# Performance work log

Measured on AMD Instinct MI355X. Metric: run time of the kernel, lower is better.

Reference implementation:

```python
import jax, jax.numpy as jnp
import numpy as np

D_MODEL = 1024
NUM_HEADS = 16
D_K = D_MODEL // NUM_HEADS
BATCH = 4
SEQ = 1024
NEG_INF = jnp.float32(-1e30)


def setup_inputs() -> dict:
    key = jax.random.key(0)
    ks = jax.random.split(key, 12)
    s = 1.0 / np.sqrt(D_MODEL)
    inp = {
        "Q": jax.random.normal(ks[0], (BATCH, SEQ, D_MODEL), jnp.float32),
        "K": jax.random.normal(ks[1], (BATCH, SEQ, D_MODEL), jnp.float32),
        "V": jax.random.normal(ks[2], (BATCH, SEQ, D_MODEL), jnp.float32),
        # causal mask, broadcastable [1,1,Sq,Sk]; entries==0 are masked out
        "mask": jnp.tril(jnp.ones((SEQ, SEQ), jnp.int32))[None, None],
        "W_q": jax.random.normal(ks[3], (D_MODEL, D_MODEL), jnp.float32) * s,
        "b_q": jnp.zeros((D_MODEL,), jnp.float32),
        "W_k": jax.random.normal(ks[4], (D_MODEL, D_MODEL), jnp.float32) * s,
        "b_k": jnp.zeros((D_MODEL,), jnp.float32),
        "W_v": jax.random.normal(ks[5], (D_MODEL, D_MODEL), jnp.float32) * s,
        "b_v": jnp.zeros((D_MODEL,), jnp.float32),
        "W_o": jax.random.normal(ks[6], (D_MODEL, D_MODEL), jnp.float32) * s,
        "b_o": jnp.zeros((D_MODEL,), jnp.float32),
    }
    return inp


def _split_heads(x):
    b, s, _ = x.shape
    return x.reshape(b, s, NUM_HEADS, D_K).transpose(0, 2, 1, 3)  # [b,h,s,dk]


def reference(Q, K, V, mask, W_q, b_q, W_k, b_k, W_v, b_v, W_o, b_o):
    # linear projections (torch Linear: x @ W.T + b)
    q = _split_heads(Q @ W_q.T + b_q)
    k = _split_heads(K @ W_k.T + b_k)
    v = _split_heads(V @ W_v.T + b_v)
    scale = 1.0 / jnp.sqrt(jnp.float32(D_K))
    scores = jnp.einsum("bhqd,bhkd->bhqk", q, k) * scale
    scores = jnp.where(mask == 0, NEG_INF, scores)
    attn = jax.nn.softmax(scores, axis=-1)  # dropout is identity in eval mode
    out = jnp.einsum("bhqk,bhkd->bhqd", attn, v)
    out = out.transpose(0, 2, 1, 3).reshape(Q.shape[0], Q.shape[1], D_MODEL)
    out = out @ W_o.T + b_o
    return out, attn
```

## Files before the change

### kernel.cpp

```cpp
#include <hip/hip_runtime.h>
#include <math.h>

#define SEQ 1024
#define DM  1024

typedef unsigned short u16;
typedef __attribute__((ext_vector_type(8))) short bf16x8;
typedef __attribute__((ext_vector_type(8))) unsigned short u16x8;
typedef __attribute__((ext_vector_type(4))) float f32x4;

__device__ __forceinline__ u16 f2bf(float f) {
  union { float f; unsigned int u; } x; x.f = f;
  return (u16)((x.u + 0x7fffu + ((x.u >> 16) & 1u)) >> 16);
}

__device__ __forceinline__ void gload16(const void* g, void* l) {
  __builtin_amdgcn_global_load_lds(
      (const __attribute__((address_space(1))) unsigned int*)g,
      (__attribute__((address_space(3))) unsigned int*)l, 16, 0, 0);
}

struct ConvArgs { const float* s[7]; u16* d[7]; };

__global__ __launch_bounds__(256) void conv_bf16(ConvArgs a) {
  const long long t  = (long long)blockIdx.x * 256 + threadIdx.x;
  const long long e0 = t * 8;
  const int u   = (int)(e0 >> 20);
  const int seg = (u < 12) ? (u >> 2) : (u - 9);
  const long long base = (u < 12) ? ((long long)(u >> 2) << 22) : ((long long)u << 20);
  const long long off  = e0 - base;
  const float* sp = a.s[seg] + off;
  float4 x = *(const float4*)sp;
  float4 y = *(const float4*)(sp + 4);
  u16x8 o;
  o[0]=f2bf(x.x); o[1]=f2bf(x.y); o[2]=f2bf(x.z); o[3]=f2bf(x.w);
  o[4]=f2bf(y.x); o[5]=f2bf(y.y); o[6]=f2bf(y.z); o[7]=f2bf(y.w);
  *(u16x8*)(a.d[seg] + off) = o;
}

struct GemmJob  { const u16* X; const u16* W; const float* bias; void* out; int mode; float scale; };
struct GemmJobs { GemmJob j[3]; };

__global__ __launch_bounds__(256) void gemm_bt(GemmJobs jobs) {
  __shared__ u16 As[8192];
  __shared__ u16 Bs[8192];
  const GemmJob job = jobs.j[blockIdx.z];
  const int tid  = threadIdx.x;
  const int wave = tid >> 6, lane = tid & 63;
  const int lm = lane & 15, qd = lane >> 4;
  const int wm = wave & 1,  wn = wave >> 1;
  const int tm = blockIdx.x * 128, tn = blockIdx.y * 128;

  f32x4 acc[4][4];
  #pragma unroll
  for (int i = 0; i < 4; i++)
    #pragma unroll
    for (int jx = 0; jx < 4; jx++) { f32x4 z = {0.f,0.f,0.f,0.f}; acc[i][jx] = z; }

  for (int kt = 0; kt < 1024; kt += 64) {
    #pragma unroll
    for (int i = 0; i < 4; i++) {
      const int s = (wave * 4 + i) * 64 + lane;
      const int r = s >> 3;
      const int c = (s & 7) ^ (r & 7);
      gload16(job.X + (size_t)(tm + r) * 1024 + kt + c * 8, As + (wave * 4 + i) * 512);
      gload16(job.W + (size_t)(tn + r) * 1024 + kt + c * 8, Bs + (wave * 4 + i) * 512);
    }
    __syncthreads();
    #pragma unroll
    for (int ks = 0; ks < 2; ks++) {
      bf16x8 af[4], bf[4];
      #pragma unroll
      for (int i = 0; i < 4; i++) {
        const int ra = wm * 64 + i * 16 + lm;
        af[i] = *(const bf16x8*)&As[ra * 64 + ((((ks << 2) | qd)) ^ (ra & 7)) * 8];
        const int rb = wn * 64 + i * 16 + lm;
        bf[i] = *(const bf16x8*)&Bs[rb * 64 + ((((ks << 2) | qd)) ^ (rb & 7)) * 8];
      }
      #pragma unroll
      for (int mi = 0; mi < 4; mi++)
        #pragma unroll
        for (int ni = 0; ni < 4; ni++)
          acc[mi][ni] = __builtin_amdgcn_mfma_f32_16x16x32_bf16(af[mi], bf[ni], acc[mi][ni], 0, 0, 0);
    }
    __syncthreads();
  }

  #pragma unroll
  for (int ni = 0; ni < 4; ni++) {
    const int n = tn + wn * 64 + ni * 16 + lm;
    const float bn = job.bias[n];
    #pragma unroll
    for (int mi = 0; mi < 4; mi++) {
      #pragma unroll
      for (int r = 0; r < 4; r++) {
        const int m = tm + wm * 64 + mi * 16 + (qd << 2) + r;
        const float v = (acc[mi][ni][r] + bn) * job.scale;
        if (job.mode == 0) {
          const int b = m >> 10, s = m & 1023, h = n >> 6, d = n & 63;
          ((u16*)job.out)[((size_t)((b << 4) + h) * 1024 + s) * 64 + d] = f2bf(v);
        } else if (job.mode == 1) {
          const int b = m >> 10, s = m & 1023, h = n >> 6, d = n & 63;
          ((u16*)job.out)[((size_t)((b << 4) + h) * 64 + d) * 1024 + s] = f2bf(v);
        } else {
          ((float*)job.out)[(size_t)m * 1024 + n] = v;
        }
      }
    }
  }
}

__global__ __launch_bounds__(256)
void attn_pass1(const u16* __restrict__ qbuf, const u16* __restrict__ kbuf,
                const u16* __restrict__ vtbuf, float* __restrict__ Linv,
                u16* __restrict__ ctx) {
  __shared__ u16 P[4][512];
  const int tid = threadIdx.x, wave = tid >> 6, lane = tid & 63;
  const int lm = lane & 15, qd = lane >> 4;
  const int qt = blockIdx.x * 4 + wave;
  const int bh = blockIdx.y;
  const int q0 = qt * 16;
  const u16* Q  = qbuf  + (size_t)bh * SEQ * 64;
  const u16* K  = kbuf  + (size_t)bh * SEQ * 64;
  const u16* VT = vtbuf + (size_t)bh * 64 * SEQ;

  const bf16x8 qa = *(const bf16x8*)(Q + (size_t)(q0 + lm) * 64 + qd * 8);
  const bf16x8 qb = *(const bf16x8*)(Q + (size_t)(q0 + lm) * 64 + 32 + qd * 8);

  f32x4 o[4];
  float lsum[4] = {0.f, 0.f, 0.f, 0.f};
  #pragma unroll
  for (int i = 0; i < 4; i++) { f32x4 z = {0.f,0.f,0.f,0.f}; o[i] = z; }
  u16* Pw = P[wave];

  for (int kt = 0; kt < q0 + 16; kt += 32) {
    const u16* k0p = K + (size_t)(kt + lm) * 64 + qd * 8;
    const u16* k1p = K + (size_t)(kt + 16 + lm) * 64 + qd * 8;
    const bf16x8 k0a = *(const bf16x8*)k0p;
    const bf16x8 k0b = *(const bf16x8*)(k0p + 32);
    const bf16x8 k1a = *(const bf16x8*)k1p;
    const bf16x8 k1b = *(const bf16x8*)(k1p + 32);
    f32x4 s0 = {0.f,0.f,0.f,0.f}, s1 = {0.f,0.f,0.f,0.f};
    s0 = __builtin_amdgcn_mfma_f32_16x16x32_bf16(qa, k0a, s0, 0, 0, 0);
    s0 = __builtin_amdgcn_mfma_f32_16x16x32_bf16(qb, k0b, s0, 0, 0, 0);
    s1 = __builtin_amdgcn_mfma_f32_16x16x32_bf16(qa, k1a, s1, 0, 0, 0);
    s1 = __builtin_amdgcn_mfma_f32_16x16x32_bf16(qb, k1b, s1, 0, 0, 0);
    #pragma unroll
    for (int r = 0; r < 4; r++) {
      const int row = q0 + (qd << 2) + r;
      const float e0 = (kt + lm      <= row) ? __expf(s0[r]) : 0.f;
      const float e1 = (kt + 16 + lm <= row) ? __expf(s1[r]) : 0.f;
      lsum[r] += e0 + e1;
      Pw[((qd << 2) + r) * 32 + lm]      = f2bf(e0);
      Pw[((qd << 2) + r) * 32 + 16 + lm] = f2bf(e1);
    }
    const bf16x8 pf = *(const bf16x8*)&Pw[lm * 32 + qd * 8];
    #pragma unroll
    for (int db = 0; db < 4; db++) {
      const bf16x8 vf = *(const bf16x8*)(VT + (size_t)(db * 16 + lm) * SEQ + kt + qd * 8);
      o[db] = __builtin_amdgcn_mfma_f32_16x16x32_bf16(pf, vf, o[db], 0, 0, 0);
    }
  }

  const int b = bh >> 4, h = bh & 15;
  #pragma unroll
  for (int r = 0; r < 4; r++) {
    float l = lsum[r];
    l += __shfl_xor(l, 1, 16);
    l += __shfl_xor(l, 2, 16);
    l += __shfl_xor(l, 4, 16);
    l += __shfl_xor(l, 8, 16);
    const float inv = 1.0f / l;
    const int row = q0 + (qd << 2) + r;
    if (lm == 0) Linv[(size_t)bh * SEQ + row] = inv;
    #pragma unroll
    for (int db = 0; db < 4; db++) {
      const int d = db * 16 + lm;
      ctx[(size_t)(b * SEQ + row) * DM + h * 64 + d] = f2bf(o[db][r] * inv);
    }
  }
}

__global__ __launch_bounds__(256)
void attn_pass2(const u16* __restrict__ qbuf, const u16* __restrict__ kbuf,
                const float* __restrict__ Linv, float* __restrict__ attn) {
  const int tid = threadIdx.x, wave = tid >> 6, lane = tid & 63;
  const int lm = lane & 15, qd = lane >> 4;
  const int bh = blockIdx.z;
  const int q0 = blockIdx.y * 64;
  const int k0 = blockIdx.x * 256 + wave * 64;
  float* A = attn + (size_t)bh * SEQ * SEQ;

  if (k0 > q0 + 63) {
    const f32x4 z = {0.f,0.f,0.f,0.f};
    #pragma unroll
    for (int i = 0; i < 16; i++)
      *(f32x4*)&A[(size_t)(q0 + i * 4 + qd) * SEQ + k0 + lm * 4] = z;
    return;
  }

  const u16* Q = qbuf + (size_t)bh * SEQ * 64;
  const u16* K = kbuf + (size_t)bh * SEQ * 64;
  bf16x8 qf[4][2]; float invl[4];
  #pragma unroll
  for (int qs = 0; qs < 4; qs++) {
    const int qq = q0 + qs * 16;
    qf[qs][0] = *(const bf16x8*)(Q + (size_t)(qq + lm) * 64 + qd * 8);
    qf[qs][1] = *(const bf16x8*)(Q + (size_t)(qq + lm) * 64 + 32 + qd * 8);
    invl[qs]  = Linv[(size_t)bh * SEQ + qq + lm];
  }
  for (int ks = 0; ks < 4; ks++) {
    const int kk = k0 + ks * 16;
    const u16* kp = K + (size_t)(kk + lm) * 64 + qd * 8;
    const bf16x8 kf0 = *(const bf16x8*)kp;
    const bf16x8 kf1 = *(const bf16x8*)(kp + 32);
    #pragma unroll
    for (int qs = 0; qs < 4; qs++) {
      const int qq = q0 + qs * 16;
      const int kbase = kk + (qd << 2);
      f32x4 v = {0.f,0.f,0.f,0.f};
      if (kk <= qq + 15) {
        f32x4 c = {0.f,0.f,0.f,0.f};
        c = __builtin_amdgcn_mfma_f32_16x16x32_bf16(kf0, qf[qs][0], c, 0, 0, 0);
        c = __builtin_amdgcn_mfma_f32_16x16x32_bf16(kf1, qf[qs][1], c, 0, 0, 0);
        const int qg = qq + lm;
        #pragma unroll
        for (int r = 0; r < 4; r++)
          v[r] = (kbase + r <= qg) ? __expf(c[r]) * invl[qs] : 0.f;
      }
      *(f32x4*)&A[(size_t)(qq + lm) * SEQ + kbase] = v;
    }
  }
}

extern "C" void kernel_launch(void* const* d_in, const int* in_sizes, int n_in,
                              void* d_out, int out_size, void* d_ws, size_t ws_size,
                              hipStream_t stream)
{
  (void)in_sizes; (void)n_in; (void)out_size; (void)ws_size;
  const float* Qf = (const float*)d_in[0];
  const float* Kf = (const float*)d_in[1];
  const float* Vf = (const float*)d_in[2];
  const float* Wq = (const float*)d_in[4];
  const float* bq = (const float*)d_in[5];
  const float* Wk = (const float*)d_in[6];
  const float* bk = (const float*)d_in[7];
  const float* Wv = (const float*)d_in[8];
  const float* bv = (const float*)d_in[9];
  const float* Wo = (const float*)d_in[10];
  const float* bo = (const float*)d_in[11];

  float* out  = (float*)d_out;
  float* attn = out + (size_t)4 * SEQ * DM;

  char* sc = (char*)attn;
  u16* Xq  = (u16*)(sc);
  u16* Xk  = (u16*)(sc + (8  << 20));
  u16* Xv  = (u16*)(sc + (16 << 20));
  u16* Wqb = (u16*)(sc + (24 << 20));
  u16* Wkb = (u16*)(sc + (26 << 20));
  u16* Wvb = (u16*)(sc + (28 << 20));
  u16* Wob = (u16*)(sc + (30 << 20));
  u16* ctx = (u16*)(sc + (32 << 20));

  char* ws   = (char*)d_ws;
  u16* qbuf  = (u16*)ws;
  u16* kbuf  = (u16*)(ws + (8  << 20));
  u16* vtbuf = (u16*)(ws + (16 << 20));
  float* Linv = (float*)(ws + (24 << 20));

  ConvArgs ca;
  ca.s[0]=Qf; ca.s[1]=Kf; ca.s[2]=Vf; ca.s[3]=Wq; ca.s[4]=Wk; ca.s[5]=Wv; ca.s[6]=Wo;
  ca.d[0]=Xq; ca.d[1]=Xk; ca.d[2]=Xv; ca.d[3]=Wqb; ca.d[4]=Wkb; ca.d[5]=Wvb; ca.d[6]=Wob;
  conv_bf16<<<8192, 256, 0, stream>>>(ca);

  GemmJobs gj;
  gj.j[0] = (GemmJob){Xq, Wqb, bq, (void*)qbuf,  0, 0.125f};
  gj.j[1] = (GemmJob){Xk, Wkb, bk, (void*)kbuf,  0, 1.0f};
  gj.j[2] = (GemmJob){Xv, Wvb, bv, (void*)vtbuf, 1, 1.0f};
  gemm_bt<<<dim3(32, 8, 3), 256, 0, stream>>>(gj);

  attn_pass1<<<dim3(16, 64), 256, 0, stream>>>(qbuf, kbuf, vtbuf, Linv, ctx);

  GemmJobs go;
  go.j[0] = (GemmJob){ctx, Wob, bo, (void*)out, 2, 1.0f};
  go.j[1] = go.j[0];
  go.j[2] = go.j[0];
  gemm_bt<<<dim3(32, 8, 1), 256, 0, stream>>>(go);

  attn_pass2<<<dim3(4, 16, 64), 256, 0, stream>>>(qbuf, kbuf, Linv, attn);
}
```

Before: 579.7 us.

## Fuse output projection GEMM and attention-probability pass into one launch

Adds a combined kernel in which the first 256 blocks compute the output projection GEMM and the remaining blocks recompute and write the normalized attention probabilities. Context and bf16 W_o move into the workspace when it is large enough, so the GEMM no longer reads from the attn output region that pass2 overwrites. This lets both jobs run in a single launch and overlap. It removes one kernel boundary and the serialization between them, at the cost of mixed block types that can load-balance unevenly, with the older two-launch path kept as a fallback.

```diff
diff --git a/kernel.cpp b/kernel.cpp
--- a/kernel.cpp
+++ b/kernel.cpp
@@ -233,11 +233,125 @@
   }
 }
 
+__global__ __launch_bounds__(256)
+void gemmo_pass2(const u16* __restrict__ ctx, const u16* __restrict__ Wob,
+                 const float* __restrict__ bo, float* __restrict__ out,
+                 const u16* __restrict__ qbuf, const u16* __restrict__ kbuf,
+                 const float* __restrict__ Linv, float* __restrict__ attn) {
+  __shared__ u16 As[8192];
+  __shared__ u16 Bs[8192];
+  const int bid = blockIdx.x;
+  const int tid = threadIdx.x, wave = tid >> 6, lane = tid & 63;
+  const int lm = lane & 15, qd = lane >> 4;
+
+  if (bid < 256) {
+    const int wm = wave & 1, wn = wave >> 1;
+    const int tm = (bid & 31) * 128, tn = (bid >> 5) * 128;
+
+    f32x4 acc[4][4];
+    #pragma unroll
+    for (int i = 0; i < 4; i++)
+      #pragma unroll
+      for (int jx = 0; jx < 4; jx++) { f32x4 z = {0.f,0.f,0.f,0.f}; acc[i][jx] = z; }
+
+    for (int kt = 0; kt < 1024; kt += 64) {
+      #pragma unroll
+      for (int i = 0; i < 4; i++) {
+        const int s = (wave * 4 + i) * 64 + lane;
+        const int r = s >> 3;
+        const int c = (s & 7) ^ (r & 7);
+        gload16(ctx + (size_t)(tm + r) * 1024 + kt + c * 8, As + (wave * 4 + i) * 512);
+        gload16(Wob + (size_t)(tn + r) * 1024 + kt + c * 8, Bs + (wave * 4 + i) * 512);
+      }
+      __syncthreads();
+      #pragma unroll
+      for (int ks = 0; ks < 2; ks++) {
+        bf16x8 af[4], bf[4];
+        #pragma unroll
+        for (int i = 0; i < 4; i++) {
+          const int ra = wm * 64 + i * 16 + lm;
+          af[i] = *(const bf16x8*)&As[ra * 64 + ((((ks << 2) | qd)) ^ (ra & 7)) * 8];
+          const int rb = wn * 64 + i * 16 + lm;
+          bf[i] = *(const bf16x8*)&Bs[rb * 64 + ((((ks << 2) | qd)) ^ (rb & 7)) * 8];
+        }
+        #pragma unroll
+        for (int mi = 0; mi < 4; mi++)
+          #pragma unroll
+          for (int ni = 0; ni < 4; ni++)
+            acc[mi][ni] = __builtin_amdgcn_mfma_f32_16x16x32_bf16(af[mi], bf[ni], acc[mi][ni], 0, 0, 0);
+      }
+      __syncthreads();
+    }
+
+    #pragma unroll
+    for (int ni = 0; ni < 4; ni++) {
+      const int n = tn + wn * 64 + ni * 16 + lm;
+      const float bn = bo[n];
+      #pragma unroll
+      for (int mi = 0; mi < 4; mi++) {
+        #pragma unroll
+        for (int r = 0; r < 4; r++) {
+          const int m = tm + wm * 64 + mi * 16 + (qd << 2) + r;
+          out[(size_t)m * 1024 + n] = acc[mi][ni][r] + bn;
+        }
+      }
+    }
+    return;
+  }
+
+  const int p  = bid - 256;
+  const int bh = p >> 6;
+  const int q0 = ((p >> 2) & 15) * 64;
+  const int k0 = (p & 3) * 256 + wave * 64;
+  float* A = attn + (size_t)bh * SEQ * SEQ;
+
+  if (k0 > q0 + 63) {
+    const f32x4 z = {0.f,0.f,0.f,0.f};
+    #pragma unroll
+    for (int i = 0; i < 16; i++)
+      *(f32x4*)&A[(size_t)(q0 + i * 4 + qd) * SEQ + k0 + lm * 4] = z;
+    return;
+  }
+
+  const u16* Q = qbuf + (size_t)bh * SEQ * 64;
+  const u16* K = kbuf + (size_t)bh * SEQ * 64;
+  bf16x8 qf[4][2]; float invl[4];
+  #pragma unroll
+  for (int qs = 0; qs < 4; qs++) {
+    const int qq = q0 + qs * 16;
+    qf[qs][0] = *(const bf16x8*)(Q + (size_t)(qq + lm) * 64 + qd * 8);
+    qf[qs][1] = *(const bf16x8*)(Q + (size_t)(qq + lm) * 64 + 32 + qd * 8);
+    invl[qs]  = Linv[(size_t)bh * SEQ + qq + lm];
+  }
+  for (int ks = 0; ks < 4; ks++) {
+    const int kk = k0 + ks * 16;
+    const u16* kp = K + (size_t)(kk + lm) * 64 + qd * 8;
+    const bf16x8 kf0 = *(const bf16x8*)kp;
+    const bf16x8 kf1 = *(const bf16x8*)(kp + 32);
+    #pragma unroll
+    for (int qs = 0; qs < 4; qs++) {
+      const int qq = q0 + qs * 16;
+      const int kbase = kk + (qd << 2);
+      f32x4 v = {0.f,0.f,0.f,0.f};
+      if (kk <= qq + 15) {
+        f32x4 c = {0.f,0.f,0.f,0.f};
+        c = __builtin_amdgcn_mfma_f32_16x16x32_bf16(kf0, qf[qs][0], c, 0, 0, 0);
+        c = __builtin_amdgcn_mfma_f32_16x16x32_bf16(kf1, qf[qs][1], c, 0, 0, 0);
+        const int qg = qq + lm;
+        #pragma unroll
+        for (int r = 0; r < 4; r++)
+          v[r] = (kbase + r <= qg) ? __expf(c[r]) * invl[qs] : 0.f;
+      }
+      *(f32x4*)&A[(size_t)(qq + lm) * SEQ + kbase] = v;
+    }
+  }
+}
+
 extern "C" void kernel_launch(void* const* d_in, const int* in_sizes, int n_in,
                               void* d_out, int out_size, void* d_ws, size_t ws_size,
                               hipStream_t stream)
 {
-  (void)in_sizes; (void)n_in; (void)out_size; (void)ws_size;
+  (void)in_sizes; (void)n_in; (void)out_size;
   const float* Qf = (const float*)d_in[0];
   const float* Kf = (const float*)d_in[1];
   const float* Vf = (const float*)d_in[2];
@@ -260,8 +374,7 @@
   u16* Wqb = (u16*)(sc + (24 << 20));
   u16* Wkb = (u16*)(sc + (26 << 20));
   u16* Wvb = (u16*)(sc + (28 << 20));
-  u16* Wob = (u16*)(sc + (30 << 20));
-  u16* ctx = (u16*)(sc + (32 << 20));
+  u16* Wob_sc = (u16*)(sc + (30 << 20));
 
   char* ws   = (char*)d_ws;
   u16* qbuf  = (u16*)ws;
@@ -269,6 +382,10 @@
   u16* vtbuf = (u16*)(ws + (16 << 20));
   float* Linv = (float*)(ws + (24 << 20));
 
+  const int big_ws = ws_size >= ((size_t)35 << 20);
+  u16* ctx = big_ws ? (u16*)(ws + (25 << 20)) : (u16*)(sc + (32 << 20));
+  u16* Wob = big_ws ? (u16*)(ws + (33 << 20)) : Wob_sc;
+
   ConvArgs ca;
   ca.s[0]=Qf; ca.s[1]=Kf; ca.s[2]=Vf; ca.s[3]=Wq; ca.s[4]=Wk; ca.s[5]=Wv; ca.s[6]=Wo;
   ca.d[0]=Xq; ca.d[1]=Xk; ca.d[2]=Xv; ca.d[3]=Wqb; ca.d[4]=Wkb; ca.d[5]=Wvb; ca.d[6]=Wob;
@@ -282,11 +399,14 @@
 
   attn_pass1<<<dim3(16, 64), 256, 0, stream>>>(qbuf, kbuf, vtbuf, Linv, ctx);
 
-  GemmJobs go;
-  go.j[0] = (GemmJob){ctx, Wob, bo, (void*)out, 2, 1.0f};
-  go.j[1] = go.j[0];
-  go.j[2] = go.j[0];
-  gemm_bt<<<dim3(32, 8, 1), 256, 0, stream>>>(go);
-
-  attn_pass2<<<dim3(4, 16, 64), 256, 0, stream>>>(qbuf, kbuf, Linv, attn);
-}
+  if (big_ws) {
+    gemmo_pass2<<<4352, 256, 0, stream>>>(ctx, Wob, bo, out, qbuf, kbuf, Linv, attn);
+  } else {
+    GemmJobs go;
+    go.j[0] = (GemmJob){ctx, Wob, bo, (void*)out, 2, 1.0f};
+    go.j[1] = go.j[0];
+    go.j[2] = go.j[0];
+    gemm_bt<<<dim3(32, 8, 1), 256, 0, stream>>>(go);
+    attn_pass2<<<dim3(4, 16, 64), 256, 0, stream>>>(qbuf, kbuf, Linv, attn);
+  }
+}
```

Result: faster. 567.4 us (-2.1%).
